# Kernel tuning notes

Hardware: AMD Instinct MI355X
Metric: run time of the kernel (lower is better)

The kernel has to match this reference:

```python
import jax, jax.numpy as jnp
import numpy as np

BATCH = 8
MAX_SEQ = 2048
HEAD_NUM = 16  # num_attention_heads_per_partition


def setup_inputs() -> dict:
    key = jax.random.key(0)
    k1, k2 = jax.random.split(key)
    attention_mask = jax.random.uniform(k1, (BATCH, 1, MAX_SEQ, MAX_SEQ), dtype=jnp.float16)
    # ragged per-sequence lengths in [1, MAX_SEQ]; concrete (shape params, not traced)
    seq_lengths = np.asarray(jax.random.randint(k2, (BATCH,), 1, MAX_SEQ + 1), dtype=np.int32)
    return {"attention_mask": attention_mask, "seq_lengths": seq_lengths}


def reference(attention_mask, seq_lengths):
    # Pack the top-left s_i x s_i block of each batch's mask, replicated across
    # HEAD_NUM heads, into one flat fp16 buffer; then threshold > 0.5 -> bool.
    mask = attention_mask.astype(jnp.float16)
    lens = [int(s) for s in np.asarray(seq_lengths)]  # static shape params
    pieces = []
    for i, s in enumerate(lens):
        block = mask[i, 0, :s, :s]                        # [s, s]
        rep = jnp.broadcast_to(block, (HEAD_NUM, s, s))   # replicate per head
        pieces.append(rep.reshape(-1))                    # [HEAD_NUM*s*s]
    packed = jnp.concatenate(pieces)                      # [sum_i HEAD_NUM*s_i^2]
    return packed > jnp.float16(0.5)
```

## Files before the change

kernel.cpp:

```cpp
#include <hip/hip_runtime.h>

#define THREADS 256
#define SRC_PER_THREAD 8
#define HEADS 16

__global__ void setup_offsets_kernel(const int* __restrict__ seq,
                                     unsigned int* __restrict__ ws) {
    if (threadIdx.x == 0 && blockIdx.x == 0) {
        unsigned int o16 = 0, os = 0;
        ws[0] = 0u; ws[9] = 0u;
        for (int b = 0; b < 8; ++b) {
            unsigned int s  = (unsigned int)seq[b];
            unsigned int s2 = s * s;
            o16 += 16u * s2;
            os  += s2;
            ws[1 + b]  = o16;
            ws[10 + b] = os;
            ws[18 + b] = s;
            ws[26 + b] = s2;
            ((float*)ws)[34 + b] = 1.0f / (float)s;
        }
    }
}

__global__ void __launch_bounds__(THREADS)
unpad_mask_kernel(const float* __restrict__ mask,
                  const unsigned int* __restrict__ ws,
                  int* __restrict__ out) {
    __shared__ unsigned int off16[9];
    __shared__ unsigned int soff[9];
    __shared__ unsigned int slen[8];
    __shared__ unsigned int ssq[8];
    __shared__ float        sinv[8];

    int tx = threadIdx.x;
    if (tx < 9) { off16[tx] = ws[tx]; soff[tx] = ws[9 + tx]; }
    if (tx < 8) {
        slen[tx] = ws[18 + tx];
        ssq[tx]  = ws[26 + tx];
        sinv[tx] = ((const float*)ws)[34 + tx];
    }
    __syncthreads();

    unsigned int total = soff[8];
    unsigned int t     = blockIdx.x * THREADS + (unsigned int)tx;
    unsigned int lane  = t & 63u;
    unsigned int wbase = (t >> 6) * (64u * SRC_PER_THREAD);
    if (wbase >= total) return;

#pragma unroll
    for (int k = 0; k < SRC_PER_THREAD; ++k) {
        unsigned int g = wbase + (unsigned int)k * 64u + lane;
        if (g >= total) break;

        unsigned int b = 0;
#pragma unroll
        for (int j = 1; j < 8; ++j) b += (g >= soff[j]) ? 1u : 0u;

        unsigned int p = g - soff[b];
        unsigned int s = slen[b];

        unsigned int row = (unsigned int)((float)p * sinv[b]);
        int col = (int)p - (int)(row * s);
        if (col < 0)            { row -= 1u; col += (int)s; }
        else if (col >= (int)s) { row += 1u; col -= (int)s; }

        float v = mask[((size_t)b << 22) + (size_t)row * 2048u + (unsigned int)col];
        int o = (v > 0.5f) ? 1 : 0;

        unsigned int s2 = ssq[b];
        int* op = out + off16[b] + p;
#pragma unroll
        for (int h = 0; h < HEADS; ++h) {
            *op = o;
            op += s2;
        }
    }
}

extern "C" void kernel_launch(void* const* d_in, const int* in_sizes, int n_in,
                              void* d_out, int out_size, void* d_ws, size_t ws_size,
                              hipStream_t stream) {
    const float*  mask = (const float*)d_in[0];
    const int*    seq  = (const int*)d_in[1];
    unsigned int* ws   = (unsigned int*)d_ws;
    int*          out  = (int*)d_out;

    setup_offsets_kernel<<<1, 64, 0, stream>>>(seq, ws);

    const unsigned int max_src   = 8u * 2048u * 2048u;
    const unsigned int per_block = THREADS * SRC_PER_THREAD;
    unsigned int blocks = (max_src + per_block - 1u) / per_block;
    unpad_mask_kernel<<<blocks, THREADS, 0, stream>>>(mask, ws, out);
}
```

Measured before the change: 751.5 us.

## Vectorize unpacked mask stores with per-batch 256-element chunks and 4 elements per lane

Reworks the work mapping so each wave processes 256-element chunks that never cross a batch boundary, with each lane handling 4 consecutive outputs. The 16 head copies are then written with int4 stores when alignment allows (even s), and mixed int4/int2/scalar stores by head phase for odd s. This aims to cut store instruction count and transaction overhead on this write-dominated kernel. The launch becomes a fixed 8192-block grid that loops over chunks. The costs are extra branching for the tail and odd-length paths, and mask loads that remain scalar.

```diff
diff --git a/kernel.cpp b/kernel.cpp
--- a/kernel.cpp
+++ b/kernel.cpp
@@ -1,21 +1,22 @@
 #include <hip/hip_runtime.h>
 
 #define THREADS 256
-#define SRC_PER_THREAD 8
-#define HEADS 16
+#define WAVES_PB 4
+#define ITERS 4
+#define MAX_BLOCKS 8192
 
 __global__ void setup_offsets_kernel(const int* __restrict__ seq,
                                      unsigned int* __restrict__ ws) {
     if (threadIdx.x == 0 && blockIdx.x == 0) {
-        unsigned int o16 = 0, os = 0;
+        unsigned int o16 = 0, cs = 0;
         ws[0] = 0u; ws[9] = 0u;
         for (int b = 0; b < 8; ++b) {
             unsigned int s  = (unsigned int)seq[b];
             unsigned int s2 = s * s;
             o16 += 16u * s2;
-            os  += s2;
+            cs  += (s2 + 255u) >> 8;
             ws[1 + b]  = o16;
-            ws[10 + b] = os;
+            ws[10 + b] = cs;
             ws[18 + b] = s;
             ws[26 + b] = s2;
             ((float*)ws)[34 + b] = 1.0f / (float)s;
@@ -28,13 +29,13 @@
                   const unsigned int* __restrict__ ws,
                   int* __restrict__ out) {
     __shared__ unsigned int off16[9];
-    __shared__ unsigned int soff[9];
+    __shared__ unsigned int csum[9];
     __shared__ unsigned int slen[8];
     __shared__ unsigned int ssq[8];
     __shared__ float        sinv[8];
 
     int tx = threadIdx.x;
-    if (tx < 9) { off16[tx] = ws[tx]; soff[tx] = ws[9 + tx]; }
+    if (tx < 9) { off16[tx] = ws[tx]; csum[tx] = ws[9 + tx]; }
     if (tx < 8) {
         slen[tx] = ws[18 + tx];
         ssq[tx]  = ws[26 + tx];
@@ -42,38 +43,93 @@
     }
     __syncthreads();
 
-    unsigned int total = soff[8];
-    unsigned int t     = blockIdx.x * THREADS + (unsigned int)tx;
-    unsigned int lane  = t & 63u;
-    unsigned int wbase = (t >> 6) * (64u * SRC_PER_THREAD);
-    if (wbase >= total) return;
+    unsigned int nchunks = csum[8];
+    unsigned int wave_id = blockIdx.x * WAVES_PB + ((unsigned int)tx >> 6);
+    unsigned int lane    = (unsigned int)tx & 63u;
 
-#pragma unroll
-    for (int k = 0; k < SRC_PER_THREAD; ++k) {
-        unsigned int g = wbase + (unsigned int)k * 64u + lane;
-        if (g >= total) break;
+#pragma unroll 1
+    for (int it = 0; it < ITERS; ++it) {
+        unsigned int chunk = wave_id * ITERS + (unsigned int)it;
+        if (chunk >= nchunks) break;
 
         unsigned int b = 0;
 #pragma unroll
-        for (int j = 1; j < 8; ++j) b += (g >= soff[j]) ? 1u : 0u;
+        for (int j = 1; j < 8; ++j) b += (chunk >= csum[j]) ? 1u : 0u;
 
-        unsigned int p = g - soff[b];
-        unsigned int s = slen[b];
+        unsigned int s    = slen[b];
+        unsigned int s2   = ssq[b];
+        float        inv  = sinv[b];
+        unsigned int p0   = (chunk - csum[b]) << 8;
+        unsigned int base = off16[b];
+        const float* mb   = mask + ((size_t)b << 22);
 
-        unsigned int row = (unsigned int)((float)p * sinv[b]);
-        int col = (int)p - (int)(row * s);
-        if (col < 0)            { row -= 1u; col += (int)s; }
-        else if (col >= (int)s) { row += 1u; col -= (int)s; }
+        if (s2 - p0 >= 256u) {
+            unsigned int q   = p0 + (lane << 2);
+            unsigned int row = (unsigned int)((float)q * inv);
+            int col = (int)q - (int)(row * s);
+            if (col < 0)            { row -= 1u; col += (int)s; }
+            else if (col >= (int)s) { row += 1u; col -= (int)s; }
 
-        float v = mask[((size_t)b << 22) + (size_t)row * 2048u + (unsigned int)col];
-        int o = (v > 0.5f) ? 1 : 0;
+            unsigned int r0 = row;  int c0 = col;
+            float v0 = mb[(size_t)r0 * 2048u + (unsigned int)c0];
+            c0++; if (c0 == (int)s) { c0 = 0; r0++; }
+            float v1 = mb[(size_t)r0 * 2048u + (unsigned int)c0];
+            c0++; if (c0 == (int)s) { c0 = 0; r0++; }
+            float v2 = mb[(size_t)r0 * 2048u + (unsigned int)c0];
+            c0++; if (c0 == (int)s) { c0 = 0; r0++; }
+            float v3 = mb[(size_t)r0 * 2048u + (unsigned int)c0];
 
-        unsigned int s2 = ssq[b];
-        int* op = out + off16[b] + p;
+            int o0 = (v0 > 0.5f) ? 1 : 0;
+            int o1 = (v1 > 0.5f) ? 1 : 0;
+            int o2 = (v2 > 0.5f) ? 1 : 0;
+            int o3 = (v3 > 0.5f) ? 1 : 0;
+            int4 o4  = make_int4(o0, o1, o2, o3);
+            int2 o2a = make_int2(o0, o1);
+            int2 o2b = make_int2(o2, o3);
+
+            if ((s & 1u) == 0u) {
+                unsigned int off = base + q;
 #pragma unroll
-        for (int h = 0; h < HEADS; ++h) {
-            *op = o;
-            op += s2;
+                for (int h = 0; h < 16; ++h) {
+                    *(int4*)(out + off) = o4;
+                    off += s2;
+                }
+            } else {
+                unsigned int off = base + q;
+#pragma unroll
+                for (int h = 0; h < 16; ++h) {
+                    if ((h & 3) == 0) {
+                        *(int4*)(out + off) = o4;
+                    } else if ((h & 3) == 2) {
+                        *(int2*)(out + off)     = o2a;
+                        *(int2*)(out + off + 2) = o2b;
+                    } else {
+                        out[off]     = o0;
+                        out[off + 1] = o1;
+                        out[off + 2] = o2;
+                        out[off + 3] = o3;
+                    }
+                    off += s2;
+                }
+            }
+        } else {
+#pragma unroll
+            for (int j = 0; j < 4; ++j) {
+                unsigned int p = p0 + (lane << 2) + (unsigned int)j;
+                if (p >= s2) continue;
+                unsigned int row = (unsigned int)((float)p * inv);
+                int col = (int)p - (int)(row * s);
+                if (col < 0)            { row -= 1u; col += (int)s; }
+                else if (col >= (int)s) { row += 1u; col -= (int)s; }
+                float v = mb[(size_t)row * 2048u + (unsigned int)col];
+                int o = (v > 0.5f) ? 1 : 0;
+                unsigned int off = base + p;
+#pragma unroll
+                for (int h = 0; h < 16; ++h) {
+                    out[off] = o;
+                    off += s2;
+                }
+            }
         }
     }
 }
@@ -87,9 +143,5 @@
     int*          out  = (int*)d_out;
 
     setup_offsets_kernel<<<1, 64, 0, stream>>>(seq, ws);
-
-    const unsigned int max_src   = 8u * 2048u * 2048u;
-    const unsigned int per_block = THREADS * SRC_PER_THREAD;
-    unsigned int blocks = (max_src + per_block - 1u) / per_block;
-    unpad_mask_kernel<<<blocks, THREADS, 0, stream>>>(mask, ws, out);
+    unpad_mask_kernel<<<MAX_BLOCKS, THREADS, 0, stream>>>(mask, ws, out);
 }
```

New measurement: 723.1 us. -3.8%, faster.
